# Optimization experiments

Hardware: AMD Instinct MI355X
Metric: run time of the kernel (lower is better)

## Reference

```python
import jax, jax.numpy as jnp
import numpy as np

N, D, NC, K = 4096, 64, 1000, 8192
ALPHA, BETA, GAMMA, SUPT = 0.02, 1.0, 1.0, 1.0
TEMP, BASE_TEMP = 0.05, 0.05
L_INTRA, L_IMEAN, L_IMIN, L_FISHER, EPS = 1.0, 0.1, 0.05, 0.1, 1e-6


def _l2norm(x, axis):
    # torch F.normalize: x / max(||x||, 1e-12)
    n = jnp.sqrt(jnp.sum(x * x, axis=axis, keepdims=True))
    return x / jnp.maximum(n, 1e-12)


def setup_inputs() -> dict:
    key = jax.random.key(0)
    k1, k2, k3, k4, k5 = jax.random.split(key, 5)
    # long-tailed class counts -> log_prior and class_weight buffers
    cls_arr = np.maximum((1280.0 * 0.01 ** (np.arange(NC) / (NC - 1))).astype(np.float32), 1.0)
    prior = cls_arr / cls_arr.sum()
    log_prior = jnp.asarray(np.log(prior), dtype=jnp.float32)
    inv = 1.0 / cls_arr
    class_weight = jnp.asarray((inv / inv.sum() * NC).astype(np.float32))
    feats = jax.random.normal(k1, (N, D), jnp.float32)
    logits = jax.random.normal(k2, (N, NC), jnp.float32)
    labels = jax.random.randint(k3, (N,), 0, NC)
    C = jax.random.normal(k4, (D, NC), jnp.float32) * 0.01  # learnable centers
    queue = jax.random.normal(k5, (K, D), jnp.float32)       # momentum queue buffer
    return {"feats": feats, "logits": logits, "labels": labels, "C": C,
            "queue": queue, "log_prior": log_prior, "class_weight": class_weight}


def reference(feats, logits, labels, C, queue, log_prior, class_weight):
    sg = jax.lax.stop_gradient
    # ---- weighted cross entropy on prior-adjusted logits ----
    sup_logits = (logits + log_prior) / SUPT
    logp = jax.nn.log_softmax(sup_logits, axis=1)
    w = class_weight[labels]
    nll = -jnp.take_along_axis(logp, labels[:, None], axis=1)[:, 0]
    ce_loss = jnp.sum(w * nll) / jnp.sum(w)

    # ---- normalize feats, enqueue (ptr=0, N<=K -> queue[:N] = feats) ----
    f = _l2norm(feats, axis=1)                       # [N, D]
    q = queue.at[:N].set(sg(f))                      # updated queue [K, D]
    centers = _l2norm(C, axis=0).T                   # [NC, D]

    neg_center_sim = f @ centers.T                   # [N, NC]
    neg_queue_sim = f @ q.T                          # [N, K]
    anchor_dot = jnp.concatenate([sg(sup_logits), neg_center_sim, neg_queue_sim], axis=1) / TEMP

    onehot = jax.nn.one_hot(labels, NC, dtype=jnp.float32)  # mask_sup == mask_cent
    mask = jnp.concatenate([onehot * BETA, onehot * ALPHA, jnp.zeros((N, K), jnp.float32)], axis=1)
    logits_mask = jnp.concatenate([jnp.ones((N, 2 * NC), jnp.float32),
                                   jnp.full((N, K), GAMMA, jnp.float32)], axis=1)

    anchor_dot = anchor_dot - sg(jnp.max(anchor_dot, axis=1, keepdims=True))
    exp_logits = jnp.exp(anchor_dot) * logits_mask
    log_prob = anchor_dot - jnp.log(jnp.sum(exp_logits, axis=1, keepdims=True) + 1e-12)
    mean_log_prob_pos = jnp.sum(mask * log_prob, axis=1) / (jnp.sum(mask, axis=1) + 1e-12)
    contrast_loss = -jnp.mean(mean_log_prob_pos) * (TEMP / BASE_TEMP)

    # ---- center regularizers ----
    gram = centers @ centers.T                       # centers are unit-norm rows
    sq = jnp.maximum(2.0 - 2.0 * gram, 1e-12)
    eye = jnp.eye(NC, dtype=bool)
    dist = jnp.sqrt(jnp.where(eye, 1e12, sq))
    dist_no_dg = jnp.where(eye, 1e6, dist)
    inter_min = jnp.min(dist_no_dg)
    inter_mean = jnp.sum(jnp.where(eye, 0.0, dist)) / (NC * (NC - 1))

    diff = f - centers[labels]                       # [N, D]
    intra_d = jnp.mean(jnp.sum(diff * diff, axis=1))
    mu_g = jnp.mean(f, axis=0, keepdims=True)
    cls_cnt = jnp.zeros((NC,), jnp.float32).at[labels].add(1.0)
    S_W = jnp.sum(diff * diff)
    S_B = jnp.sum(jnp.sum((centers - mu_g) ** 2, axis=1) * cls_cnt)
    fisher = S_B / (S_W + EPS)
    reg = (L_INTRA * intra_d + L_IMEAN / (inter_mean + EPS)
           + L_IMIN / (inter_min + EPS) + L_FISHER / (fisher + EPS))
    return ce_loss + contrast_loss + reg
```

## Files before the change

kernel.cpp:

```cpp
#include <hip/hip_runtime.h>
#include <math.h>

#define N_ 4096
#define D_ 64
#define NC_ 1000
#define KQ_ 8192
#define VCOLS 9192
#define VPAD  9216
#define PCH   73
#define TEMP_INV 20.0f
#define M0 20.25f
#define LOG2E 1.4426950408889634f
#define K2L  (TEMP_INV * LOG2E)
#define M0L  (M0 * LOG2E)

#define WS_F     0
#define WS_CENT  (WS_F + N_*D_)
#define WS_SUPM  (WS_CENT + NC_*D_)
#define WS_PSUP  (WS_SUPM + N_)
#define WS_PCENT (WS_PSUP + N_)
#define WS_CEPN  (WS_PCENT + N_)
#define WS_CEPD  (WS_CEPN + 1024)
#define WS_CSP   (WS_CEPD + 1024)
#define WS_GS    (WS_CSP + 16)
#define WS_GM    (WS_GS + 128)
#define WS_VF    (WS_GM + 128)
#define WS_VC    (WS_VF + 4096)
#define WS_TP    (WS_VC + 4096)
#define WS_CTR   (WS_TP + 64)
#define WS_PS    (WS_CTR + 4)
#define WS_BBF   (WS_PS + N_*PCH)

#define K1_BLOCKS 2058
#define K2_BLOCKS 5824
#define K3_BLOCKS 16

typedef __attribute__((ext_vector_type(8))) short short8_t;
typedef __attribute__((ext_vector_type(4))) float f32x4;

__device__ __forceinline__ ushort f2bf(float x) {
    union { float f; unsigned u; } v; v.f = x;
    unsigned r = (v.u + 0x7FFFu + ((v.u >> 16) & 1u)) >> 16;
    return (ushort)r;
}

__device__ __forceinline__ int swz(int byte) {
    return byte ^ (((byte >> 7) & 7) << 4);
}

__global__ __launch_bounds__(256) void k1(const float* __restrict__ feats,
                                          const float* __restrict__ C,
                                          const float* __restrict__ queue,
                                          float* __restrict__ ws,
                                          ushort* __restrict__ B) {
    int b = blockIdx.x;
    int t = threadIdx.x;
    if (b == 0 && t == 0) ((unsigned*)ws)[WS_CTR] = 0u;
    if (b < 1024) {
        int row  = b * 4 + (t >> 6);
        int lane = t & 63;
        float x = feats[row * D_ + lane];
        float ss = x * x;
        #pragma unroll
        for (int m = 32; m >= 1; m >>= 1) ss += __shfl_xor(ss, m, 64);
        float y = x / fmaxf(sqrtf(ss), 1e-12f);
        ws[WS_F + row * D_ + lane] = y;
        B[(size_t)(NC_ + row) * D_ + lane] = f2bf(y);
    } else if (b < 1028) {
        int c = (b - 1024) * 256 + t;
        if (c >= NC_) return;
        float v[D_];
        float ss = 0.0f;
        #pragma unroll
        for (int d = 0; d < D_; ++d) { float x = C[d * NC_ + c]; v[d] = x; ss += x * x; }
        float inv = 1.0f / fmaxf(sqrtf(ss), 1e-12f);
        #pragma unroll
        for (int d = 0; d < D_; ++d) {
            float y = v[d] * inv;
            ws[WS_CENT + c * D_ + d] = y;
            B[(size_t)c * D_ + d] = f2bf(y);
        }
    } else {
        int q = (b - 1028) * 256 + t;
        if (q >= (KQ_ - N_ + 24) * D_) return;
        int r = q >> 6, d = q & 63;
        ushort o = 0;
        if (r < KQ_ - N_) o = f2bf(queue[(size_t)(N_ + r) * D_ + d]);
        B[(size_t)(NC_ + N_ + r) * D_ + d] = o;
    }
}

__global__ __launch_bounds__(256) void k2(const ushort* __restrict__ B,
                                          const float* __restrict__ logits,
                                          const int* __restrict__ labels,
                                          const float* __restrict__ log_prior,
                                          const float* __restrict__ class_weight,
                                          const float* __restrict__ f,
                                          const float* __restrict__ cent,
                                          float* __restrict__ ws) {
    __shared__ char smem[25600];
    int t = threadIdx.x;
    int l = t & 63, w = t >> 6;
    int bid = blockIdx.x;
    int wm = w >> 1, wn = w & 1;
    int lr = l & 15, lg = l >> 4;
    int lk = lg * 8;

    if (bid >= 1216) {
        char* AtC = smem;
        char* BtC = smem + 8192;
        float (*ssum)[2] = (float(*)[2])(smem + 24576);

        int g = bid - 1216;
        int cg = g >> 6;
        int bx = g & 63;
        int r0 = bx * 64;
        int c0 = cg * 128;

        const short8_t* Ag8 = (const short8_t*)(B + (size_t)(NC_ + r0) * D_);
        const short8_t* Bg8 = (const short8_t*)(B + (size_t)c0 * D_);
        #pragma unroll
        for (int i = 0; i < 2; ++i) {
            int cid = t + i * 256;
            *(short8_t*)(AtC + swz(cid * 16)) = Ag8[cid];
        }
        #pragma unroll
        for (int i = 0; i < 4; ++i) {
            int cid = t + i * 256;
            *(short8_t*)(BtC + swz(cid * 16)) = Bg8[cid];
        }
        __syncthreads();

        short8_t a[2][2], bfr[4][2];
        #pragma unroll
        for (int rf = 0; rf < 2; ++rf) {
            int row = wm * 32 + rf * 16 + lr;
            #pragma unroll
            for (int ks = 0; ks < 2; ++ks)
                a[rf][ks] = *(const short8_t*)(AtC + swz(row * 128 + ks * 64 + lg * 16));
        }
        #pragma unroll
        for (int cf = 0; cf < 4; ++cf) {
            int col = wn * 64 + cf * 16 + lr;
            #pragma unroll
            for (int ks = 0; ks < 2; ++ks)
                bfr[cf][ks] = *(const short8_t*)(BtC + swz(col * 128 + ks * 64 + lg * 16));
        }

        f32x4 acc[2][4] = {};
        #pragma unroll
        for (int ks = 0; ks < 2; ++ks)
            #pragma unroll
            for (int rf = 0; rf < 2; ++rf)
                #pragma unroll
                for (int cf = 0; cf < 4; ++cf)
                    acc[rf][cf] = __builtin_amdgcn_mfma_f32_16x16x32_bf16(
                        a[rf][ks], bfr[cf][ks], acc[rf][cf], 0, 0, 0);

        if (c0 < NC_) {
            #pragma unroll
            for (int rf = 0; rf < 2; ++rf)
                #pragma unroll
                for (int reg = 0; reg < 4; ++reg) {
                    int row = r0 + wm * 32 + rf * 16 + lg * 4 + reg;
                    int lab = labels[row];
                    #pragma unroll
                    for (int cf = 0; cf < 4; ++cf) {
                        int col = c0 + wn * 64 + cf * 16 + lr;
                        if (col == lab) ws[WS_PCENT + row] = acc[rf][cf][reg];
                    }
                }
        }

        #pragma unroll
        for (int rf = 0; rf < 2; ++rf) {
            float se[4] = {0, 0, 0, 0};
            #pragma unroll
            for (int cf = 0; cf < 4; ++cf)
                #pragma unroll
                for (int reg = 0; reg < 4; ++reg)
                    se[reg] += __builtin_amdgcn_exp2f(
                        fmaf(acc[rf][cf][reg], K2L, -M0L));
            #pragma unroll
            for (int reg = 0; reg < 4; ++reg) {
                float v = se[reg];
                #pragma unroll
                for (int msk = 1; msk < 16; msk <<= 1)
                    v += __shfl_xor(v, msk, 64);
                if (lr == 0) ssum[wm * 32 + rf * 16 + lg * 4 + reg][wn] = v;
            }
        }
        __syncthreads();
        if (t < 64)
            ws[WS_PS + (size_t)(r0 + t) * PCH + cg] = ssum[t][0] + ssum[t][1];
    } else if (bid < 1024) {
        float* lp = (float*)smem;
        float (*cep)[2] = (float(*)[2])(smem + 4096);
        if (t < 250) ((float4*)lp)[t] = ((const float4*)log_prior)[t];
        __syncthreads();
        int row = bid * 4 + w;
        const float* lrow = logits + (size_t)row * NC_;
        const float4* lrow4 = (const float4*)lrow;
        float vals[16];
        float m = -1e30f;
        #pragma unroll
        for (int it = 0; it < 4; ++it) {
            int idx = it * 64 + l;
            float4 v4 = (idx < 250) ? lrow4[idx]
                                    : make_float4(-1e30f, -1e30f, -1e30f, -1e30f);
            float4 p4 = (idx < 250) ? ((const float4*)lp)[idx]
                                    : make_float4(0, 0, 0, 0);
            vals[it * 4 + 0] = v4.x + p4.x;
            vals[it * 4 + 1] = v4.y + p4.y;
            vals[it * 4 + 2] = v4.z + p4.z;
            vals[it * 4 + 3] = v4.w + p4.w;
            #pragma unroll
            for (int k = 0; k < 4; ++k) m = fmaxf(m, vals[it * 4 + k]);
        }
        #pragma unroll
        for (int msk = 1; msk < 64; msk <<= 1) m = fmaxf(m, __shfl_xor(m, msk, 64));
        float s1 = 0.0f, s20 = 0.0f;
        #pragma unroll
        for (int k = 0; k < 16; ++k) {
            float d = vals[k] - m;
            s1  += __builtin_amdgcn_exp2f(d * LOG2E);
            s20 += __builtin_amdgcn_exp2f(d * K2L);
        }
        #pragma unroll
        for (int msk = 1; msk < 64; msk <<= 1) {
            s1  += __shfl_xor(s1, msk, 64);
            s20 += __shfl_xor(s20, msk, 64);
        }
        if (l == 0) {
            int lab = labels[row];
            float vpos = lrow[lab] + lp[lab];
            float wt = class_weight[lab];
            cep[w][0] = wt * (m + __logf(s1) - vpos);
            cep[w][1] = wt;
            ws[WS_SUPM + row] = TEMP_INV * m;
            ws[WS_PS + (size_t)row * PCH + (PCH - 1)] = s20;
            ws[WS_PSUP + row] = TEMP_INV * vpos;
        }
        __syncthreads();
        if (t == 0) {
            ws[WS_CEPN + bid] = cep[0][0] + cep[1][0] + cep[2][0] + cep[3][0];
            ws[WS_CEPD + bid] = cep[0][1] + cep[1][1] + cep[2][1] + cep[3][1];
        }
    } else if (bid < 1152) {
        float* gs4 = (float*)smem;
        float* gm4 = gs4 + 4;
        int g = bid - 1024;
        int gr = g >> 3, gc = g & 7;
        int r0 = gr * 64 + wm * 32;
        int c0 = gc * 128 + wn * 64;

        const ushort* Af = B + (size_t)(r0 + lr) * D_ + lk;
        const ushort* Bf = B + (size_t)(c0 + lr) * D_ + lk;

        short8_t a[2][2], bfr[4][2];
        #pragma unroll
        for (int rf = 0; rf < 2; ++rf)
            #pragma unroll
            for (int ks = 0; ks < 2; ++ks)
                a[rf][ks] = *(const short8_t*)(Af + rf * 16 * D_ + ks * 32);
        #pragma unroll
        for (int cf = 0; cf < 4; ++cf)
            #pragma unroll
            for (int ks = 0; ks < 2; ++ks)
                bfr[cf][ks] = *(const short8_t*)(Bf + cf * 16 * D_ + ks * 32);

        f32x4 acc[2][4] = {};
        #pragma unroll
        for (int ks = 0; ks < 2; ++ks)
            #pragma unroll
            for (int rf = 0; rf < 2; ++rf)
                #pragma unroll
                for (int cf = 0; cf < 4; ++cf)
                    acc[rf][cf] = __builtin_amdgcn_mfma_f32_16x16x32_bf16(
                        a[rf][ks], bfr[cf][ks], acc[rf][cf], 0, 0, 0);

        float lsum = 0.0f, lmin = 1e30f;
        #pragma unroll
        for (int rf = 0; rf < 2; ++rf)
            #pragma unroll
            for (int cf = 0; cf < 4; ++cf)
                #pragma unroll
                for (int reg = 0; reg < 4; ++reg) {
                    int gi = r0 + rf * 16 + lg * 4 + reg;
                    int gj = c0 + cf * 16 + lr;
                    if (gi < NC_ && gj < NC_ && gi != gj) {
                        float d = sqrtf(fmaxf(2.0f - 2.0f * acc[rf][cf][reg], 1e-12f));
                        lsum += d;
                        lmin = fminf(lmin, d);
                    }
                }
        #pragma unroll
        for (int msk = 1; msk < 64; msk <<= 1) {
            lsum += __shfl_xor(lsum, msk, 64);
            lmin = fminf(lmin, __shfl_xor(lmin, msk, 64));
        }
        if (l == 0) { gs4[w] = lsum; gm4[w] = lmin; }
        __syncthreads();
        if (t == 0) {
            ws[WS_GS + g] = gs4[0] + gs4[1] + gs4[2] + gs4[3];
            ws[WS_GM + g] = fminf(fminf(gm4[0], gm4[1]), fminf(gm4[2], gm4[3]));
        }
    } else {
        float* svf = (float*)smem;
        float* svc = svf + 256;
        float* stp = svc + 256;
        int sb = bid - 1152;
        int wid = sb * 4 + w;
        float vf = 0.0f, vc = 0.0f, tacc = 0.0f;
        for (int i = wid; i < N_; i += 256) {
            float x = f[i * D_ + l];
            float c = cent[labels[i] * D_ + l];
            vf += x; vc += c; tacc += x * c;
        }
        #pragma unroll
        for (int msk = 32; msk >= 1; msk >>= 1) tacc += __shfl_xor(tacc, msk, 64);
        svf[w * 64 + l] = vf; svc[w * 64 + l] = vc;
        if (l == 0) stp[w] = tacc;
        __syncthreads();
        if (w == 0) {
            ws[WS_VF + sb * 64 + l] = svf[l] + svf[64 + l] + svf[128 + l] + svf[192 + l];
            ws[WS_VC + sb * 64 + l] = svc[l] + svc[64 + l] + svc[128 + l] + svc[192 + l];
            if (l == 0) ws[WS_TP + sb] = stp[0] + stp[1] + stp[2] + stp[3];
        }
    }
}

__global__ __launch_bounds__(256) void k3(float* __restrict__ ws,
                                          float* __restrict__ out) {
    int t = threadIdx.x;
    int w = t >> 6, l = t & 63;
    int bid = blockIdx.x;
    __shared__ unsigned done;
    __shared__ float cb[4];

    {
        int row = bid * 256 + t;
        const float* pv = ws + WS_PS + (size_t)row * PCH;
        float s = 0.0f;
        #pragma unroll
        for (int c = 0; c < PCH - 1; ++c) s += pv[c];
        float msup = ws[WS_SUPM + row];
        float ssup = pv[PCH - 1];
        float M = fmaxf(M0, msup);
        float stot = s * __builtin_amdgcn_exp2f((M0 - M) * LOG2E)
                   + ssup * __builtin_amdgcn_exp2f((msup - M) * LOG2E);
        float logS = __logf(stot + 1e-12f);
        float lp1 = ws[WS_PSUP + row] - M - logS;
        float lp2 = ws[WS_PCENT + row] * TEMP_INV - M - logS;
        float cacc = (lp1 + 0.02f * lp2) / (1.02f + 1e-12f);
        #pragma unroll
        for (int msk = 1; msk < 64; msk <<= 1) cacc += __shfl_xor(cacc, msk, 64);
        if (l == 0) cb[w] = cacc;
        __syncthreads();
        if (t == 0) ws[WS_CSP + bid] = cb[0] + cb[1] + cb[2] + cb[3];
    }

    __threadfence();
    if (t == 0) done = atomicAdd((unsigned*)ws + WS_CTR, 1u);
    __syncthreads();
    if (done != K3_BLOCKS - 1) return;
    __threadfence();

    float csum = (t < 16) ? ws[WS_CSP + t] : 0.0f;
    float cen = 0.0f, ced = 0.0f;
    #pragma unroll
    for (int k = 0; k < 4; ++k) {
        cen += ws[WS_CEPN + t + k * 256];
        ced += ws[WS_CEPD + t + k * 256];
    }
    float gsum = 0, gmin = 1e30f, vf = 0, vc = 0, tp = 0;
    if (t < 64) {
        tp = ws[WS_TP + t];
        #pragma unroll 8
        for (int b = 0; b < 64; ++b) {
            vf += ws[WS_VF + b * 64 + t];
            vc += ws[WS_VC + b * 64 + t];
        }
    }
    if (t < 128) { gsum = ws[WS_GS + t]; gmin = ws[WS_GM + t]; }
    float mu_d = vf * (1.0f / (float)N_);
    float vmu  = vc * mu_d;
    float mumu = mu_d * mu_d;
    #pragma unroll
    for (int m = 32; m >= 1; m >>= 1) {
        csum += __shfl_xor(csum, m, 64);
        cen  += __shfl_xor(cen, m, 64);
        ced  += __shfl_xor(ced, m, 64);
        gsum += __shfl_xor(gsum, m, 64);
        gmin = fminf(gmin, __shfl_xor(gmin, m, 64));
        vmu  += __shfl_xor(vmu, m, 64);
        mumu += __shfl_xor(mumu, m, 64);
        tp   += __shfl_xor(tp, m, 64);
    }
    __shared__ float red[4][8];
    if (l == 0) {
        red[w][0] = csum; red[w][1] = cen; red[w][2] = ced; red[w][3] = gsum;
        red[w][4] = gmin; red[w][5] = vmu; red[w][6] = mumu; red[w][7] = tp;
    }
    __syncthreads();
    if (t == 0) {
        float CSM = red[0][0] + red[1][0] + red[2][0] + red[3][0];
        float CEN = red[0][1] + red[1][1] + red[2][1] + red[3][1];
        float CED = red[0][2] + red[1][2] + red[2][2] + red[3][2];
        float GSM = red[0][3] + red[1][3] + red[2][3] + red[3][3];
        float GMN = fminf(fminf(red[0][4], red[1][4]), fminf(red[2][4], red[3][4]));
        float VMU = red[0][5] + red[1][5] + red[2][5] + red[3][5];
        float MUMU = red[0][6] + red[1][6] + red[2][6] + red[3][6];
        float T   = red[0][7] + red[1][7] + red[2][7] + red[3][7];
        float SW = 2.0f * (float)N_ - 2.0f * T;
        float SB = (float)N_ - 2.0f * VMU + (float)N_ * MUMU;
        float intra = SW / (float)N_;
        float fisher = SB / (SW + 1e-6f);
        float ce = CEN / CED;
        float contrast = -(CSM / (float)N_);
        float inter_mean = GSM / (float)(NC_ * (NC_ - 1));
        float reg = intra + 0.1f / (inter_mean + 1e-6f)
                  + 0.05f / (GMN + 1e-6f) + 0.1f / (fisher + 1e-6f);
        out[0] = ce + contrast + reg;
    }
}

extern "C" void kernel_launch(void* const* d_in, const int* in_sizes, int n_in,
                              void* d_out, int out_size, void* d_ws, size_t ws_size,
                              hipStream_t stream) {
    const float* feats        = (const float*)d_in[0];
    const float* logits       = (const float*)d_in[1];
    const int*   labels       = (const int*)d_in[2];
    const float* C            = (const float*)d_in[3];
    const float* queue        = (const float*)d_in[4];
    const float* log_prior    = (const float*)d_in[5];
    const float* class_weight = (const float*)d_in[6];
    float* ws  = (float*)d_ws;
    float* out = (float*)d_out;
    ushort* Bbf = (ushort*)(ws + WS_BBF);

    hipLaunchKernelGGL(k1, dim3(K1_BLOCKS), dim3(256), 0, stream,
                       feats, C, queue, ws, Bbf);
    hipLaunchKernelGGL(k2, dim3(K2_BLOCKS), dim3(256), 0, stream,
                       Bbf, logits, labels, log_prior, class_weight,
                       ws + WS_F, ws + WS_CENT, ws);
    hipLaunchKernelGGL(k3, dim3(K3_BLOCKS), dim3(256), 0, stream, ws, out);
}
```

Before: 43.69 us.

## Loop each GEMM block over four row tiles with double-buffered A in LDS

The contrastive GEMM blocks now each keep one 128-column B tile resident and iterate over four 64-row A tiles. The next A tile is prefetched into registers and then written into a second LDS buffer while the current tile is processed, which raises B reuse and cuts the block count from 4608 to 1152. Block-index ranges for the other roles are remapped to match. The trade-offs are less parallelism per launch, larger LDS use per block and more serial work per block, which could lower occupancy.

```diff
diff --git a/kernel.cpp b/kernel.cpp
--- a/kernel.cpp
+++ b/kernel.cpp
@@ -32,7 +32,7 @@
 #define WS_BBF   (WS_PS + N_*PCH)
 
 #define K1_BLOCKS 2058
-#define K2_BLOCKS 5824
+#define K2_BLOCKS 2368
 #define K3_BLOCKS 16
 
 typedef __attribute__((ext_vector_type(8))) short short8_t;
@@ -98,7 +98,7 @@
                                           const float* __restrict__ f,
                                           const float* __restrict__ cent,
                                           float* __restrict__ ws) {
-    __shared__ char smem[25600];
+    __shared__ char smem[34816];
     int t = threadIdx.x;
     int l = t & 63, w = t >> 6;
     int bid = blockIdx.x;
@@ -106,39 +106,34 @@
     int lr = l & 15, lg = l >> 4;
     int lk = lg * 8;
 
-    if (bid >= 1216) {
-        char* AtC = smem;
-        char* BtC = smem + 8192;
-        float (*ssum)[2] = (float(*)[2])(smem + 24576);
-
-        int g = bid - 1216;
-        int cg = g >> 6;
-        int bx = g & 63;
-        int r0 = bx * 64;
+    if (bid >= 1024 && bid < 2176) {
+        char* BtC  = smem;
+        char* At0C = smem + 16384;
+        char* At1C = smem + 24576;
+        float (*ssum4)[64][2] = (float(*)[64][2])(smem + 32768);
+
+        int g = bid - 1024;
+        int cg = g >> 4;
+        int rg = g & 15;
         int c0 = cg * 128;
-
-        const short8_t* Ag8 = (const short8_t*)(B + (size_t)(NC_ + r0) * D_);
+        int rbase = rg * 256;
+        bool doext = (c0 < NC_);
+
         const short8_t* Bg8 = (const short8_t*)(B + (size_t)c0 * D_);
-        #pragma unroll
-        for (int i = 0; i < 2; ++i) {
-            int cid = t + i * 256;
-            *(short8_t*)(AtC + swz(cid * 16)) = Ag8[cid];
-        }
-        #pragma unroll
-        for (int i = 0; i < 4; ++i) {
-            int cid = t + i * 256;
-            *(short8_t*)(BtC + swz(cid * 16)) = Bg8[cid];
-        }
-        __syncthreads();
-
-        short8_t a[2][2], bfr[4][2];
-        #pragma unroll
-        for (int rf = 0; rf < 2; ++rf) {
-            int row = wm * 32 + rf * 16 + lr;
-            #pragma unroll
-            for (int ks = 0; ks < 2; ++ks)
-                a[rf][ks] = *(const short8_t*)(AtC + swz(row * 128 + ks * 64 + lg * 16));
-        }
+        const short8_t* Ag8 = (const short8_t*)(B + (size_t)(NC_ + rbase) * D_);
+
+        short8_t bReg0 = Bg8[t], bReg1 = Bg8[t + 256],
+                 bReg2 = Bg8[t + 512], bReg3 = Bg8[t + 768];
+        short8_t aReg0 = Ag8[t], aReg1 = Ag8[t + 256];
+        *(short8_t*)(BtC + swz((t      ) * 16)) = bReg0;
+        *(short8_t*)(BtC + swz((t +  256) * 16)) = bReg1;
+        *(short8_t*)(BtC + swz((t +  512) * 16)) = bReg2;
+        *(short8_t*)(BtC + swz((t +  768) * 16)) = bReg3;
+        *(short8_t*)(At0C + swz((t      ) * 16)) = aReg0;
+        *(short8_t*)(At0C + swz((t + 256) * 16)) = aReg1;
+        __syncthreads();
+
+        short8_t bfr[4][2];
         #pragma unroll
         for (int cf = 0; cf < 4; ++cf) {
             int col = wn * 64 + cf * 16 + lr;
@@ -147,52 +142,78 @@
                 bfr[cf][ks] = *(const short8_t*)(BtC + swz(col * 128 + ks * 64 + lg * 16));
         }
 
-        f32x4 acc[2][4] = {};
-        #pragma unroll
-        for (int ks = 0; ks < 2; ++ks)
-            #pragma unroll
-            for (int rf = 0; rf < 2; ++rf)
+        #pragma unroll
+        for (int it = 0; it < 4; ++it) {
+            if (it < 3) {
+                aReg0 = Ag8[(it + 1) * 512 + t];
+                aReg1 = Ag8[(it + 1) * 512 + t + 256];
+            }
+            const char* AcurC = (it & 1) ? At1C : At0C;
+            char* AnxtC = (it & 1) ? At0C : At1C;
+
+            short8_t a[2][2];
+            #pragma unroll
+            for (int rf = 0; rf < 2; ++rf) {
+                int row = wm * 32 + rf * 16 + lr;
+                #pragma unroll
+                for (int ks = 0; ks < 2; ++ks)
+                    a[rf][ks] = *(const short8_t*)(AcurC + swz(row * 128 + ks * 64 + lg * 16));
+            }
+
+            f32x4 acc[2][4] = {};
+            #pragma unroll
+            for (int ks = 0; ks < 2; ++ks)
+                #pragma unroll
+                for (int rf = 0; rf < 2; ++rf)
+                    #pragma unroll
+                    for (int cf = 0; cf < 4; ++cf)
+                        acc[rf][cf] = __builtin_amdgcn_mfma_f32_16x16x32_bf16(
+                            a[rf][ks], bfr[cf][ks], acc[rf][cf], 0, 0, 0);
+
+            if (doext) {
+                #pragma unroll
+                for (int rf = 0; rf < 2; ++rf)
+                    #pragma unroll
+                    for (int reg = 0; reg < 4; ++reg) {
+                        int row = rbase + it * 64 + wm * 32 + rf * 16 + lg * 4 + reg;
+                        int lab = labels[row];
+                        #pragma unroll
+                        for (int cf = 0; cf < 4; ++cf) {
+                            int col = c0 + wn * 64 + cf * 16 + lr;
+                            if (col == lab) ws[WS_PCENT + row] = acc[rf][cf][reg];
+                        }
+                    }
+            }
+
+            #pragma unroll
+            for (int rf = 0; rf < 2; ++rf) {
+                float se[4] = {0, 0, 0, 0};
                 #pragma unroll
                 for (int cf = 0; cf < 4; ++cf)
-                    acc[rf][cf] = __builtin_amdgcn_mfma_f32_16x16x32_bf16(
-                        a[rf][ks], bfr[cf][ks], acc[rf][cf], 0, 0, 0);
-
-        if (c0 < NC_) {
-            #pragma unroll
-            for (int rf = 0; rf < 2; ++rf)
+                    #pragma unroll
+                    for (int reg = 0; reg < 4; ++reg)
+                        se[reg] += __builtin_amdgcn_exp2f(
+                            fmaf(acc[rf][cf][reg], K2L, -M0L));
                 #pragma unroll
                 for (int reg = 0; reg < 4; ++reg) {
-                    int row = r0 + wm * 32 + rf * 16 + lg * 4 + reg;
-                    int lab = labels[row];
+                    float v = se[reg];
                     #pragma unroll
-                    for (int cf = 0; cf < 4; ++cf) {
-                        int col = c0 + wn * 64 + cf * 16 + lr;
-                        if (col == lab) ws[WS_PCENT + row] = acc[rf][cf][reg];
-                    }
+                    for (int msk = 1; msk < 16; msk <<= 1)
+                        v += __shfl_xor(v, msk, 64);
+                    if (lr == 0) ssum4[it][wm * 32 + rf * 16 + lg * 4 + reg][wn] = v;
                 }
-        }
-
-        #pragma unroll
-        for (int rf = 0; rf < 2; ++rf) {
-            float se[4] = {0, 0, 0, 0};
-            #pragma unroll
-            for (int cf = 0; cf < 4; ++cf)
-                #pragma unroll
-                for (int reg = 0; reg < 4; ++reg)
-                    se[reg] += __builtin_amdgcn_exp2f(
-                        fmaf(acc[rf][cf][reg], K2L, -M0L));
-            #pragma unroll
-            for (int reg = 0; reg < 4; ++reg) {
-                float v = se[reg];
-                #pragma unroll
-                for (int msk = 1; msk < 16; msk <<= 1)
-                    v += __shfl_xor(v, msk, 64);
-                if (lr == 0) ssum[wm * 32 + rf * 16 + lg * 4 + reg][wn] = v;
-            }
-        }
-        __syncthreads();
-        if (t < 64)
-            ws[WS_PS + (size_t)(r0 + t) * PCH + cg] = ssum[t][0] + ssum[t][1];
+            }
+
+            if (it < 3) {
+                *(short8_t*)(AnxtC + swz((t      ) * 16)) = aReg0;
+                *(short8_t*)(AnxtC + swz((t + 256) * 16)) = aReg1;
+            }
+            __syncthreads();
+            if (t < 64) {
+                int row = rbase + it * 64 + t;
+                ws[WS_PS + (size_t)row * PCH + cg] = ssum4[it][t][0] + ssum4[it][t][1];
+            }
+        }
     } else if (bid < 1024) {
         float* lp = (float*)smem;
         float (*cep)[2] = (float(*)[2])(smem + 4096);
@@ -246,10 +267,10 @@
             ws[WS_CEPN + bid] = cep[0][0] + cep[1][0] + cep[2][0] + cep[3][0];
             ws[WS_CEPD + bid] = cep[0][1] + cep[1][1] + cep[2][1] + cep[3][1];
         }
-    } else if (bid < 1152) {
+    } else if (bid < 2304) {
         float* gs4 = (float*)smem;
         float* gm4 = gs4 + 4;
-        int g = bid - 1024;
+        int g = bid - 2176;
         int gr = g >> 3, gc = g & 7;
         int r0 = gr * 64 + wm * 32;
         int c0 = gc * 128 + wn * 64;
@@ -309,7 +330,7 @@
         float* svf = (float*)smem;
         float* svc = svf + 256;
         float* stp = svc + 256;
-        int sb = bid - 1152;
+        int sb = bid - 2304;
         int wid = sb * 4 + w;
         float vf = 0.0f, vc = 0.0f, tacc = 0.0f;
         for (int i = wid; i < N_; i += 256) {
```

Measured after the change: 45.09 us. 1.03x slower.

## Make contrastive GEMM blocks persistent with double-buffered async LDS loads

Applied to the files above, without the earlier changes.

The exp-sum GEMM blocks used to be one block per 64x128 tile, 4608 blocks in all. Now 256 blocks each loop over 18 column tiles. A register-resident A tile is reused across tiles, and B tiles are double-buffered through direct global-to-LDS loads so the next tile loads while the current one is computed. Exp sums are accumulated in registers, so the per-row partial-sum array shrinks from 73 to 5 entries and the final reduction reads fewer values. This trades parallelism (fewer blocks, each with a serial loop and a barrier per step) for less launch and staging overhead and better data reuse.

```diff
diff --git a/kernel.cpp b/kernel.cpp
--- a/kernel.cpp
+++ b/kernel.cpp
@@ -7,7 +7,7 @@
 #define KQ_ 8192
 #define VCOLS 9192
 #define VPAD  9216
-#define PCH   73
+#define PCH   5
 #define TEMP_INV 20.0f
 #define M0 20.25f
 #define LOG2E 1.4426950408889634f
@@ -32,7 +32,7 @@
 #define WS_BBF   (WS_PS + N_*PCH)
 
 #define K1_BLOCKS 2058
-#define K2_BLOCKS 5824
+#define K2_BLOCKS 1472
 #define K3_BLOCKS 16
 
 typedef __attribute__((ext_vector_type(8))) short short8_t;
@@ -46,6 +46,12 @@
 
 __device__ __forceinline__ int swz(int byte) {
     return byte ^ (((byte >> 7) & 7) << 4);
+}
+
+__device__ __forceinline__ void gload16(const void* g, void* lds) {
+    __builtin_amdgcn_global_load_lds(
+        (const __attribute__((address_space(1))) unsigned int*)g,
+        (__attribute__((address_space(3))) unsigned int*)lds, 16, 0, 0);
 }
 
 __global__ __launch_bounds__(256) void k1(const float* __restrict__ feats,
@@ -98,7 +104,7 @@
                                           const float* __restrict__ f,
                                           const float* __restrict__ cent,
                                           float* __restrict__ ws) {
-    __shared__ char smem[25600];
+    __shared__ char smem[33280];
     int t = threadIdx.x;
     int l = t & 63, w = t >> 6;
     int bid = blockIdx.x;
@@ -106,99 +112,131 @@
     int lr = l & 15, lg = l >> 4;
     int lk = lg * 8;
 
-    if (bid >= 1216) {
-        char* AtC = smem;
-        char* BtC = smem + 8192;
-        float (*ssum)[2] = (float(*)[2])(smem + 24576);
-
-        int g = bid - 1216;
-        int cg = g >> 6;
-        int bx = g & 63;
+    if (bid < 256) {
+        char* buf0 = smem;
+        char* buf1 = smem + 16384;
+        float (*ssum)[2] = (float(*)[2])(smem + 32768);
+
+        int bx = bid & 63, cg = bid >> 6;
         int r0 = bx * 64;
-        int c0 = cg * 128;
-
-        const short8_t* Ag8 = (const short8_t*)(B + (size_t)(NC_ + r0) * D_);
-        const short8_t* Bg8 = (const short8_t*)(B + (size_t)c0 * D_);
-        #pragma unroll
-        for (int i = 0; i < 2; ++i) {
-            int cid = t + i * 256;
-            *(short8_t*)(AtC + swz(cid * 16)) = Ag8[cid];
-        }
-        #pragma unroll
-        for (int i = 0; i < 4; ++i) {
-            int cid = t + i * 256;
-            *(short8_t*)(BtC + swz(cid * 16)) = Bg8[cid];
-        }
-        __syncthreads();
-
-        short8_t a[2][2], bfr[4][2];
+        int cbase = cg * 2304;
+
+        const char* Ag = (const char*)(B + (size_t)(NC_ + r0) * D_);
+        #pragma unroll
+        for (int j = 0; j < 2; ++j) {
+            int seg = w * 2 + j;
+            int o = seg * 64 + l;
+            int sc = o ^ ((o >> 3) & 7);
+            gload16(Ag + sc * 16, buf0 + seg * 1024);
+        }
+        __syncthreads();
+        short8_t a[2][2];
         #pragma unroll
         for (int rf = 0; rf < 2; ++rf) {
             int row = wm * 32 + rf * 16 + lr;
             #pragma unroll
             for (int ks = 0; ks < 2; ++ks)
-                a[rf][ks] = *(const short8_t*)(AtC + swz(row * 128 + ks * 64 + lg * 16));
-        }
-        #pragma unroll
-        for (int cf = 0; cf < 4; ++cf) {
-            int col = wn * 64 + cf * 16 + lr;
+                a[rf][ks] = *(const short8_t*)(buf0 + swz(row * 128 + ks * 64 + lg * 16));
+        }
+        __syncthreads();
+
+        int lab[2][4];
+        if (cg == 0) {
+            #pragma unroll
+            for (int rf = 0; rf < 2; ++rf)
+                #pragma unroll
+                for (int reg = 0; reg < 4; ++reg)
+                    lab[rf][reg] = labels[r0 + wm * 32 + rf * 16 + lg * 4 + reg];
+        }
+
+        const char* Bg = (const char*)(B + (size_t)cbase * D_);
+        auto stageB = [&](int tile, char* buf) {
+            const char* Bt = Bg + (size_t)tile * 16384;
+            #pragma unroll
+            for (int j = 0; j < 4; ++j) {
+                int seg = w * 4 + j;
+                int o = seg * 64 + l;
+                int sc = o ^ ((o >> 3) & 7);
+                gload16(Bt + sc * 16, buf + seg * 1024);
+            }
+        };
+
+        stageB(0, buf0);
+        __syncthreads();
+
+        float se[2][4] = {};
+        #pragma unroll 2
+        for (int it = 0; it < 18; ++it) {
+            char* cur = (it & 1) ? buf1 : buf0;
+            char* nxt = (it & 1) ? buf0 : buf1;
+            if (it < 17) stageB(it + 1, nxt);
+
+            short8_t bfr[4][2];
+            #pragma unroll
+            for (int cf = 0; cf < 4; ++cf) {
+                int col = wn * 64 + cf * 16 + lr;
+                #pragma unroll
+                for (int ks = 0; ks < 2; ++ks)
+                    bfr[cf][ks] = *(const short8_t*)(cur + swz(col * 128 + ks * 64 + lg * 16));
+            }
+
+            f32x4 acc[2][4] = {};
             #pragma unroll
             for (int ks = 0; ks < 2; ++ks)
-                bfr[cf][ks] = *(const short8_t*)(BtC + swz(col * 128 + ks * 64 + lg * 16));
-        }
-
-        f32x4 acc[2][4] = {};
-        #pragma unroll
-        for (int ks = 0; ks < 2; ++ks)
+                #pragma unroll
+                for (int rf = 0; rf < 2; ++rf)
+                    #pragma unroll
+                    for (int cf = 0; cf < 4; ++cf)
+                        acc[rf][cf] = __builtin_amdgcn_mfma_f32_16x16x32_bf16(
+                            a[rf][ks], bfr[cf][ks], acc[rf][cf], 0, 0, 0);
+
+            if (cg == 0 && it < 8) {
+                #pragma unroll
+                for (int rf = 0; rf < 2; ++rf)
+                    #pragma unroll
+                    for (int reg = 0; reg < 4; ++reg) {
+                        #pragma unroll
+                        for (int cf = 0; cf < 4; ++cf) {
+                            int col = it * 128 + wn * 64 + cf * 16 + lr;
+                            if (col == lab[rf][reg])
+                                ws[WS_PCENT + r0 + wm * 32 + rf * 16 + lg * 4 + reg] =
+                                    acc[rf][cf][reg];
+                        }
+                    }
+            }
+
             #pragma unroll
             for (int rf = 0; rf < 2; ++rf)
                 #pragma unroll
                 for (int cf = 0; cf < 4; ++cf)
-                    acc[rf][cf] = __builtin_amdgcn_mfma_f32_16x16x32_bf16(
-                        a[rf][ks], bfr[cf][ks], acc[rf][cf], 0, 0, 0);
-
-        if (c0 < NC_) {
-            #pragma unroll
-            for (int rf = 0; rf < 2; ++rf)
-                #pragma unroll
-                for (int reg = 0; reg < 4; ++reg) {
-                    int row = r0 + wm * 32 + rf * 16 + lg * 4 + reg;
-                    int lab = labels[row];
                     #pragma unroll
-                    for (int cf = 0; cf < 4; ++cf) {
-                        int col = c0 + wn * 64 + cf * 16 + lr;
-                        if (col == lab) ws[WS_PCENT + row] = acc[rf][cf][reg];
-                    }
-                }
-        }
-
-        #pragma unroll
-        for (int rf = 0; rf < 2; ++rf) {
-            float se[4] = {0, 0, 0, 0};
-            #pragma unroll
-            for (int cf = 0; cf < 4; ++cf)
-                #pragma unroll
-                for (int reg = 0; reg < 4; ++reg)
-                    se[reg] += __builtin_amdgcn_exp2f(
-                        fmaf(acc[rf][cf][reg], K2L, -M0L));
+                    for (int reg = 0; reg < 4; ++reg)
+                        se[rf][reg] += __builtin_amdgcn_exp2f(
+                            fmaf(acc[rf][cf][reg], K2L, -M0L));
+
+            __syncthreads();
+        }
+
+        #pragma unroll
+        for (int rf = 0; rf < 2; ++rf)
             #pragma unroll
             for (int reg = 0; reg < 4; ++reg) {
-                float v = se[reg];
+                float v = se[rf][reg];
                 #pragma unroll
                 for (int msk = 1; msk < 16; msk <<= 1)
                     v += __shfl_xor(v, msk, 64);
                 if (lr == 0) ssum[wm * 32 + rf * 16 + lg * 4 + reg][wn] = v;
             }
-        }
         __syncthreads();
         if (t < 64)
             ws[WS_PS + (size_t)(r0 + t) * PCH + cg] = ssum[t][0] + ssum[t][1];
-    } else if (bid < 1024) {
+    } else if (bid < 1280) {
         float* lp = (float*)smem;
         float (*cep)[2] = (float(*)[2])(smem + 4096);
+        int sid = bid - 256;
         if (t < 250) ((float4*)lp)[t] = ((const float4*)log_prior)[t];
         __syncthreads();
-        int row = bid * 4 + w;
+        int row = sid * 4 + w;
         const float* lrow = logits + (size_t)row * NC_;
         const float4* lrow4 = (const float4*)lrow;
         float vals[16];
@@ -243,13 +281,13 @@
         }
         __syncthreads();
         if (t == 0) {
-            ws[WS_CEPN + bid] = cep[0][0] + cep[1][0] + cep[2][0] + cep[3][0];
-            ws[WS_CEPD + bid] = cep[0][1] + cep[1][1] + cep[2][1] + cep[3][1];
-        }
-    } else if (bid < 1152) {
+            ws[WS_CEPN + sid] = cep[0][0] + cep[1][0] + cep[2][0] + cep[3][0];
+            ws[WS_CEPD + sid] = cep[0][1] + cep[1][1] + cep[2][1] + cep[3][1];
+        }
+    } else if (bid < 1408) {
         float* gs4 = (float*)smem;
         float* gm4 = gs4 + 4;
-        int g = bid - 1024;
+        int g = bid - 1280;
         int gr = g >> 3, gc = g & 7;
         int r0 = gr * 64 + wm * 32;
         int c0 = gc * 128 + wn * 64;
@@ -309,7 +347,7 @@
         float* svf = (float*)smem;
         float* svc = svf + 256;
         float* stp = svc + 256;
-        int sb = bid - 1152;
+        int sb = bid - 1408;
         int wid = sb * 4 + w;
         float vf = 0.0f, vc = 0.0f, tacc = 0.0f;
         for (int i = wid; i < N_; i += 256) {
@@ -341,9 +379,7 @@
     {
         int row = bid * 256 + t;
         const float* pv = ws + WS_PS + (size_t)row * PCH;
-        float s = 0.0f;
-        #pragma unroll
-        for (int c = 0; c < PCH - 1; ++c) s += pv[c];
+        float s = (pv[0] + pv[1]) + (pv[2] + pv[3]);
         float msup = ws[WS_SUPM + row];
         float ssup = pv[PCH - 1];
         float M = fmaxf(M0, msup);
```

Result: faster. 41.50 us (-5.0%).
